# Kernel tuning notes

Hardware: AMD Instinct MI355X
Metric: run time of the kernel (lower is better)

## Reference

```python
import jax, jax.numpy as jnp
import numpy as np

# Dimensions (see shape_source): batch, tokens, input dim, attention feature dim, output dim
B, T, D_IN, D_ATTN, D_OUT = 8, 2048, 512, 8, 512
# Weight scale keeps Q,K entries ~N(0, 0.5^2) so scores**power stays finite in fp32
W_SCALE = 0.5 / np.sqrt(D_IN)


def setup_inputs() -> dict:
    key = jax.random.key(0)
    k1, k2, k3, k4 = jax.random.split(key, 4)
    Input = jax.random.normal(k1, (B, T, D_IN), dtype=jnp.float32)
    W_q = jax.random.normal(k2, (D_IN, D_ATTN), dtype=jnp.float32) * W_SCALE
    W_k = jax.random.normal(k3, (D_IN, D_ATTN), dtype=jnp.float32) * W_SCALE
    W_v = jax.random.normal(k4, (D_IN, D_OUT), dtype=jnp.float32) * W_SCALE
    return {"Input": Input, "W_q": W_q, "W_k": W_k, "W_v": W_v, "power": D_ATTN}


def reference(Input, W_q, W_k, W_v, power):
    # QKV projections (torch.mm applied per token)
    Q = jnp.einsum('btd,df->btf', Input, W_q)   # [B,T,D_ATTN]
    K = jnp.einsum('btd,df->btf', Input, W_k)   # [B,T,D_ATTN]
    V = jnp.einsum('btd,do->bto', Input, W_v)   # [B,T,D_OUT]
    # Non-standard score transform: elementwise power by Attention.Feature.Num
    scores = jnp.einsum('btf,bsf->bts', Q, K) ** power  # [B,T,T]
    A = jax.nn.softmax(scores, axis=2)
    # Weighted sum of values
    return jnp.einsum('bts,bso->bto', A, V)  # [B,T,D_OUT]
```

## Files before the change

kernel.cpp:

```cpp
#include <hip/hip_runtime.h>
#include <hip/hip_bf16.h>
#include <stdint.h>


typedef float f32x4_t __attribute__((ext_vector_type(4)));
typedef short s16x8_t __attribute__((ext_vector_type(8)));
typedef unsigned int u32;

static __device__ __forceinline__ unsigned short f2bf(float x){
  union { float f; u32 u; } v; v.f = x;
  return (unsigned short)((v.u + 0x7FFFu + ((v.u >> 16) & 1u)) >> 16);
}

static __device__ __forceinline__ u32 pk2bf(float a, float b){
  __hip_bfloat162 h = __float22bfloat162_rn(float2{a, b});
  union { __hip_bfloat162 h2; u32 u; } c; c.h2 = h;
  return c.u;
}

static __device__ __forceinline__ void gload16(const void* g, void* l){
  __builtin_amdgcn_global_load_lds((const __attribute__((address_space(1))) u32*)g,
                                   (__attribute__((address_space(3))) u32*)l, 16, 0, 0);
}

static __device__ __forceinline__ float dot8(const float* q, const float4& a, const float4& b){
  float s = q[0] * a.x;
  s = fmaf(q[1], a.y, s); s = fmaf(q[2], a.z, s); s = fmaf(q[3], a.w, s);
  s = fmaf(q[4], b.x, s); s = fmaf(q[5], b.y, s); s = fmaf(q[6], b.z, s);
  s = fmaf(q[7], b.w, s);
  return s;
}

__global__ __launch_bounds__(256) void k_wvT(const float* __restrict__ Wv,
                                             unsigned short* __restrict__ WvT){
  __shared__ __align__(16) float tile[64][68];
  const int t = threadIdx.x;
  const int dbase = (blockIdx.x >> 3) * 64;
  const int cbase = (blockIdx.x & 7) * 64;
  {
    const int dl = t >> 2, cq = (t & 3) * 16;
    const float* src = Wv + (size_t)(dbase + dl) * 512 + cbase + cq;
#pragma unroll
    for (int i = 0; i < 16; i += 4){
      float4 v = *(const float4*)(src + i);
      tile[dl][cq + i + 0] = v.x; tile[dl][cq + i + 1] = v.y;
      tile[dl][cq + i + 2] = v.z; tile[dl][cq + i + 3] = v.w;
    }
  }
  __syncthreads();
  const int cl = t >> 2, dq = (t & 3) * 16;
  __align__(16) unsigned short o[16];
#pragma unroll
  for (int i = 0; i < 16; ++i) o[i] = f2bf(tile[dq + i][cl]);
  unsigned short* dst = WvT + (size_t)(cbase + cl) * 512 + dbase + dq;
  *(uint4*)dst = *(const uint4*)o;
  *(uint4*)(dst + 8) = *(const uint4*)(o + 8);
}

__global__ __launch_bounds__(256) void k_fused(const float* __restrict__ In,
                                               const float* __restrict__ Wq,
                                               const float* __restrict__ Wk,
                                               const unsigned short* __restrict__ WvT,
                                               float* __restrict__ Qo,
                                               float* __restrict__ Ko,
                                               unsigned short* __restrict__ Vg){
  __shared__ __align__(16) char smem[65536];
  const int t = threadIdx.x;
  if (blockIdx.x < 1024){
    float* wt = (float*)smem;
#pragma unroll
    for (int i = 0; i < 16; i += 4){
      float4 vq = *(const float4*)(Wq + t * 16 + i);
      float4 vk = *(const float4*)(Wk + t * 16 + i);
      const float* pq = &vq.x;
      const float* pk = &vk.x;
#pragma unroll
      for (int j = 0; j < 4; ++j){
        int flat = t * 16 + i + j;
        int d = flat >> 3, f = flat & 7;
        wt[f * 512 + ((((d >> 2) ^ f) << 2) | (d & 3))] = pq[j];
        int fk = f + 8;
        wt[fk * 512 + ((((d >> 2) ^ (fk & 7)) << 2) | (d & 3))] = pk[j];
      }
    }
    __syncthreads();
    const int tok = (int)blockIdx.x * 16 + (t >> 4);
    const int f = t & 15;
    const float* inrow = In + (size_t)tok * 512;
    const float* wrow = &wt[f * 512];
    const int swz = f & 7;
    double acc = 0.0;
    for (int cb = 0; cb < 128; cb += 8){
      float part = 0.f;
#pragma unroll
      for (int c = cb; c < cb + 8; ++c){
        float4 x = *(const float4*)(inrow + c * 4);
        float4 ww = *(const float4*)(wrow + ((c ^ swz) << 2));
        part = fmaf(x.x, ww.x, part); part = fmaf(x.y, ww.y, part);
        part = fmaf(x.z, ww.z, part); part = fmaf(x.w, ww.w, part);
      }
      acc += (double)part;
    }
    float r = (float)acc;
    if (f < 8) Qo[(size_t)tok * 8 + f] = r;
    else       Ko[(size_t)tok * 8 + (f - 8)] = r;
    return;
  }
  char* Ab = smem;
  char* Bb = smem + 16384;
  char* Img = smem + 32768;
  const int vb = (int)blockIdx.x - 1024;
  const int w = t >> 6, lane = t & 63;
  const int mt = vb >> 2, nt = vb & 3;
  const int wm = w >> 1, wn = w & 1;
  const int asub = lane & 3;
  int arow[2], acr[2];
#pragma unroll
  for (int i = 0; i < 2; ++i){
    arow[i] = (w * 2 + i) * 16 + (lane >> 2);
    acr[i]  = asub ^ ((arow[i] >> 1) & 3);
  }
  f32x4_t acc[4][4];
#pragma unroll
  for (int m = 0; m < 4; ++m)
#pragma unroll
    for (int n = 0; n < 4; ++n)
      acc[m][n] = (f32x4_t){0.f, 0.f, 0.f, 0.f};

  auto stageB = [&](int kk, int sel){
#pragma unroll
    for (int i = 0; i < 2; ++i){
      int id = w * 2 + i;
      const unsigned short* gb = WvT + (size_t)(nt * 128 + arow[i]) * 512 + kk * 32 + acr[i] * 8;
      gload16(gb, Bb + sel * 8192 + id * 1024);
    }
  };
  auto loadA = [&](int kk, float4* x, float4* y){
#pragma unroll
    for (int i = 0; i < 2; ++i){
      const float* ga = In + (size_t)(mt * 128 + arow[i]) * 512 + kk * 32 + acr[i] * 8;
      x[i] = *(const float4*)ga;
      y[i] = *(const float4*)(ga + 4);
    }
  };
  auto writeA = [&](const float4* x, const float4* y, int sel){
#pragma unroll
    for (int i = 0; i < 2; ++i){
      __align__(16) unsigned short pk[8] = {
        f2bf(x[i].x), f2bf(x[i].y), f2bf(x[i].z), f2bf(x[i].w),
        f2bf(y[i].x), f2bf(y[i].y), f2bf(y[i].z), f2bf(y[i].w)};
      *(uint4*)(Ab + sel * 8192 + arow[i] * 64 + asub * 16) = *(const uint4*)pk;
    }
  };
  {
    float4 x[2], y[2];
    loadA(0, x, y);
    stageB(0, 0);
    writeA(x, y, 0);
    __syncthreads();
  }
  for (int kk = 0; kk < 16; ++kk){
    const int cur = kk & 1;
    float4 x[2], y[2];
    if (kk < 15){
      loadA(kk + 1, x, y);
      stageB(kk + 1, cur ^ 1);
    }
    s16x8_t a[4], bf[4];
#pragma unroll
    for (int m = 0; m < 4; ++m){
      int row = wm * 64 + m * 16 + (lane & 15);
      int chn = (lane >> 4) ^ ((row >> 1) & 3);
      a[m] = *(const s16x8_t*)(Ab + cur * 8192 + row * 64 + chn * 16);
    }
#pragma unroll
    for (int n = 0; n < 4; ++n){
      int col = wn * 64 + n * 16 + (lane & 15);
      int chn = (lane >> 4) ^ ((col >> 1) & 3);
      bf[n] = *(const s16x8_t*)(Bb + cur * 8192 + col * 64 + chn * 16);
    }
#pragma unroll
    for (int m = 0; m < 4; ++m)
#pragma unroll
      for (int n = 0; n < 4; ++n)
        acc[m][n] = __builtin_amdgcn_mfma_f32_16x16x32_bf16(a[m], bf[n], acc[m][n], 0, 0, 0);
    if (kk < 15) writeA(x, y, cur ^ 1);
    __syncthreads();
  }
#pragma unroll
  for (int m = 0; m < 4; ++m){
    const int ks2 = (wm * 2 + (m >> 1)) & 3;
    const int hi  = (m * 2 + ((lane >> 4) >> 1)) & 3;
    const int lo0 = ((lane >> 4) & 1) * 4;
#pragma unroll
    for (int n = 0; n < 4; ++n){
      const int g_loc = wn * 2 + (n >> 1);
      const int n2 = n & 1;
      const int cl = lane & 15;
      __align__(8) unsigned short pk2[4];
#pragma unroll
      for (int j = 0; j < 4; ++j) pk2[j] = f2bf(acc[m][n][j]);
      int boff = g_loc * 8192 + n2 * 4096 + ks2 * 1024 + hi * 256 + cl * 16 + lo0 * 2;
      *(uint2*)(Img + boff) = *(const uint2*)pk2;
    }
  }
  __syncthreads();
  const int bq = mt >> 4;
  const int kt = mt & 15;
#pragma unroll
  for (int i = 0; i < 8; ++i){
    int G = i * 256 + t;
    unsigned short* dst = Vg + (size_t)bq * 1048576 + (size_t)kt * 65536
                        + nt * 16384 + G * 8;
    *(uint4*)dst = *(const uint4*)(Img + G * 16);
  }
}

__global__ __launch_bounds__(1024) void k_attn(const float* __restrict__ Qg,
                                               const float* __restrict__ Kg,
                                               const unsigned short* __restrict__ Vg,
                                               float* __restrict__ Out){
  __shared__ __align__(16) char smem[102656];
  const int t = threadIdx.x;
  const int g = t >> 6, lane = t & 63;
  const int b = blockIdx.x & 7;
  const int qt = blockIdx.x >> 3;
  const int qbase = qt * 64;

  float qreg[8];
  {
    const float* Qp = Qg + (size_t)(b * 2048 + qbase + lane) * 8;
    float4 a = *(const float4*)Qp;
    float4 c = *(const float4*)(Qp + 4);
    qreg[0] = a.x; qreg[1] = a.y; qreg[2] = a.z; qreg[3] = a.w;
    qreg[4] = c.x; qreg[5] = c.y; qreg[6] = c.z; qreg[7] = c.w;
  }
  const float* Kp = Kg + (size_t)b * (2048 * 8);
  const unsigned short* Vb = Vg + (size_t)b * 1048576;
  char* Klds = smem;
  char* Pb = smem + 65536;
  float* red = (float*)(smem + 98304);
  float* fin = (float*)(smem + 102400);

#pragma unroll
  for (int i = 0; i < 4; ++i)
    gload16(Kp + (size_t)(i * 1024 + t) * 4, Klds + (i * 1024 + t) * 16);
  __syncthreads();

  float amax = 0.f;
  {
    const float* kbase = (const float*)Klds + (g * 8) * 8;
#pragma unroll 2
    for (int tt = 0; tt < 16; ++tt){
      const float* kb = kbase + tt * 1024;
#pragma unroll
      for (int j = 0; j < 8; ++j){
        float4 k0 = *(const float4*)(kb + j * 8);
        float4 k1 = *(const float4*)(kb + j * 8 + 4);
        amax = fmaxf(amax, fabsf(dot8(qreg, k0, k1)));
      }
    }
  }
  red[g * 64 + lane] = amax;
  __syncthreads();
  float am = red[lane];
#pragma unroll
  for (int s = 1; s < 16; ++s) am = fmaxf(am, red[s * 64 + lane]);
  float mreg;
  { float s2 = am * am; float s4 = s2 * s2; mreg = s4 * s4; }
  const float LOG2E = 1.44269504f;
  const float me2 = mreg * LOG2E;
  float lp = 0.f;

  const int pswz = ((g ^ (lane & 15)) << 4);
  auto score = [&](int tt, int sel){
    const float* kb = (const float*)Klds + (tt * 128 + g * 8) * 8;
    float es[8];
#pragma unroll
    for (int j = 0; j < 8; ++j){
      float4 k0 = *(const float4*)(kb + j * 8);
      float4 k1 = *(const float4*)(kb + j * 8 + 4);
      float s = dot8(qreg, k0, k1);
      float s2 = s * s; float s4 = s2 * s2; float p = s4 * s4;
      es[j] = exp2f(fmaf(p, LOG2E, -me2));
      lp += es[j];
    }
    uint4 pkd;
    pkd.x = pk2bf(es[0], es[1]); pkd.y = pk2bf(es[2], es[3]);
    pkd.z = pk2bf(es[4], es[5]); pkd.w = pk2bf(es[6], es[7]);
    *(uint4*)(Pb + sel * 16384 + lane * 256 + pswz) = pkd;
  };

  f32x4_t acc[4][2];
#pragma unroll
  for (int mm = 0; mm < 4; ++mm)
#pragma unroll
    for (int n = 0; n < 2; ++n)
      acc[mm][n] = (f32x4_t){0.f, 0.f, 0.f, 0.f};

  score(0, 0);
  __syncthreads();

  for (int tt = 0; tt < 16; ++tt){
    const int sel = tt & 1;
    s16x8_t vf[2][4];
    {
      const unsigned short* vb = Vb + (size_t)tt * 65536 + g * 4096 + lane * 8;
#pragma unroll
      for (int n = 0; n < 2; ++n)
#pragma unroll
        for (int ks = 0; ks < 4; ++ks)
          vf[n][ks] = *(const s16x8_t*)(vb + n * 2048 + ks * 512);
    }
    if (tt + 1 < 16) score(tt + 1, sel ^ 1);
#pragma unroll
    for (int ks = 0; ks < 4; ++ks){
      s16x8_t a[4];
#pragma unroll
      for (int mm = 0; mm < 4; ++mm){
        int r = mm * 16 + (lane & 15);
        int slot = (ks * 4 + (lane >> 4)) ^ (r & 15);
        a[mm] = *(const s16x8_t*)(Pb + sel * 16384 + r * 256 + (slot << 4));
      }
      __builtin_amdgcn_s_setprio(1);
#pragma unroll
      for (int mm = 0; mm < 4; ++mm)
#pragma unroll
        for (int n = 0; n < 2; ++n)
          acc[mm][n] = __builtin_amdgcn_mfma_f32_16x16x32_bf16(a[mm], vf[n][ks], acc[mm][n], 0, 0, 0);
      __builtin_amdgcn_s_setprio(0);
    }
    __syncthreads();
  }

  red[g * 64 + lane] = lp;
  __syncthreads();
  if (t < 64){
    float s = red[t];
#pragma unroll
    for (int s2 = 1; s2 < 16; ++s2) s += red[s2 * 64 + t];
    fin[t] = 1.f / s;
  }
  __syncthreads();

  float* img = (float*)smem;
#pragma unroll
  for (int mm = 0; mm < 4; ++mm){
    float linv[4];
#pragma unroll
    for (int j = 0; j < 4; ++j)
      linv[j] = fin[mm * 16 + ((lane >> 4) << 2) + j];
#pragma unroll
    for (int n = 0; n < 2; ++n){
      int colL = g * 32 + n * 16 + (lane & 15);
#pragma unroll
      for (int j = 0; j < 4; ++j){
        int r16 = ((lane >> 4) << 2) + j;
        img[r16 * 520 + colL] = acc[mm][n][j] * linv[j];
      }
    }
    __syncthreads();
#pragma unroll
    for (int i = 0; i < 2; ++i){
      int f4 = i * 1024 + t;
      int r16 = f4 >> 7, c4 = f4 & 127;
      float4 v = *(const float4*)(img + r16 * 520 + c4 * 4);
      *(float4*)(Out + (size_t)(b * 2048 + qbase + mm * 16 + r16) * 512 + c4 * 4) = v;
    }
    __syncthreads();
  }
}

extern "C" void kernel_launch(void* const* d_in, const int* in_sizes, int n_in,
                              void* d_out, int out_size, void* d_ws, size_t ws_size,
                              hipStream_t stream){
  const float* In = (const float*)d_in[0];
  const float* Wq = (const float*)d_in[1];
  const float* Wk = (const float*)d_in[2];
  const float* Wv = (const float*)d_in[3];
  char* ws = (char*)d_ws;
  unsigned short* WvT = (unsigned short*)(ws);
  float* Q            = (float*)(ws + 524288);
  float* K            = (float*)(ws + 1048576);
  unsigned short* Vg  = (unsigned short*)(ws + 1572864);
  float* Out = (float*)d_out;

  hipLaunchKernelGGL(k_wvT,   dim3(64),   dim3(256),  0, stream, Wv, WvT);
  hipLaunchKernelGGL(k_fused, dim3(1536), dim3(256),  0, stream, In, Wq, Wk, WvT, Q, K, Vg);
  hipLaunchKernelGGL(k_attn,  dim3(256),  dim3(1024), 0, stream, Q, K, Vg, Out);
}
```

Baseline: 102.5 us.

## Double-buffer V fragment loads across tiles and stage input rows in LDS

The attention loop now prefetches the next tile's V fragments into a second register buffer, unrolled by two, so global V loads overlap the current tile's MFMA work instead of being issued right before it. The QK projection blocks copy their 16 input rows into LDS asynchronously and compute from there instead of reading global memory per thread. The max-score pass tracks s*s instead of |s|, which saves one squaring later. More live vector registers may lower occupancy.

```diff
diff --git a/kernel.cpp b/kernel.cpp
--- a/kernel.cpp
+++ b/kernel.cpp
@@ -68,6 +68,11 @@
   const int t = threadIdx.x;
   if (blockIdx.x < 1024){
     float* wt = (float*)smem;
+    float* inT = (float*)(smem + 32768);
+    const float* Inb = In + (size_t)blockIdx.x * 16 * 512;
+#pragma unroll
+    for (int i = 0; i < 8; ++i)
+      gload16(Inb + (i * 256 + t) * 4, (char*)inT + (i * 256 + t) * 16);
 #pragma unroll
     for (int i = 0; i < 16; i += 4){
       float4 vq = *(const float4*)(Wq + t * 16 + i);
@@ -84,9 +89,9 @@
       }
     }
     __syncthreads();
-    const int tok = (int)blockIdx.x * 16 + (t >> 4);
+    const int tokl = t >> 4;
     const int f = t & 15;
-    const float* inrow = In + (size_t)tok * 512;
+    const float* inrow = inT + tokl * 512;
     const float* wrow = &wt[f * 512];
     const int swz = f & 7;
     double acc = 0.0;
@@ -102,6 +107,7 @@
       acc += (double)part;
     }
     float r = (float)acc;
+    const int tok = (int)blockIdx.x * 16 + tokl;
     if (f < 8) Qo[(size_t)tok * 8 + f] = r;
     else       Ko[(size_t)tok * 8 + (f - 8)] = r;
     return;
@@ -247,7 +253,7 @@
     gload16(Kp + (size_t)(i * 1024 + t) * 4, Klds + (i * 1024 + t) * 16);
   __syncthreads();
 
-  float amax = 0.f;
+  float amax2 = 0.f;
   {
     const float* kbase = (const float*)Klds + (g * 8) * 8;
 #pragma unroll 2
@@ -257,17 +263,18 @@
       for (int j = 0; j < 8; ++j){
         float4 k0 = *(const float4*)(kb + j * 8);
         float4 k1 = *(const float4*)(kb + j * 8 + 4);
-        amax = fmaxf(amax, fabsf(dot8(qreg, k0, k1)));
+        float s = dot8(qreg, k0, k1);
+        amax2 = fmaxf(amax2, s * s);
       }
     }
   }
-  red[g * 64 + lane] = amax;
+  red[g * 64 + lane] = amax2;
   __syncthreads();
   float am = red[lane];
 #pragma unroll
   for (int s = 1; s < 16; ++s) am = fmaxf(am, red[s * 64 + lane]);
   float mreg;
-  { float s2 = am * am; float s4 = s2 * s2; mreg = s4 * s4; }
+  { float s4 = am * am; mreg = s4 * s4; }
   const float LOG2E = 1.44269504f;
   const float me2 = mreg * LOG2E;
   float lp = 0.f;
@@ -291,6 +298,15 @@
     *(uint4*)(Pb + sel * 16384 + lane * 256 + pswz) = pkd;
   };
 
+  auto vload = [&](int tt, s16x8_t vf[2][4]){
+    const unsigned short* vb = Vb + (size_t)tt * 65536 + g * 4096 + lane * 8;
+#pragma unroll
+    for (int n = 0; n < 2; ++n)
+#pragma unroll
+      for (int ks = 0; ks < 4; ++ks)
+        vf[n][ks] = *(const s16x8_t*)(vb + n * 2048 + ks * 512);
+  };
+
   f32x4_t acc[4][2];
 #pragma unroll
   for (int mm = 0; mm < 4; ++mm)
@@ -298,21 +314,7 @@
     for (int n = 0; n < 2; ++n)
       acc[mm][n] = (f32x4_t){0.f, 0.f, 0.f, 0.f};
 
-  score(0, 0);
-  __syncthreads();
-
-  for (int tt = 0; tt < 16; ++tt){
-    const int sel = tt & 1;
-    s16x8_t vf[2][4];
-    {
-      const unsigned short* vb = Vb + (size_t)tt * 65536 + g * 4096 + lane * 8;
-#pragma unroll
-      for (int n = 0; n < 2; ++n)
-#pragma unroll
-        for (int ks = 0; ks < 4; ++ks)
-          vf[n][ks] = *(const s16x8_t*)(vb + n * 2048 + ks * 512);
-    }
-    if (tt + 1 < 16) score(tt + 1, sel ^ 1);
+  auto mfma_tile = [&](int sel, s16x8_t vf[2][4]){
 #pragma unroll
     for (int ks = 0; ks < 4; ++ks){
       s16x8_t a[4];
@@ -330,6 +332,24 @@
           acc[mm][n] = __builtin_amdgcn_mfma_f32_16x16x32_bf16(a[mm], vf[n][ks], acc[mm][n], 0, 0, 0);
       __builtin_amdgcn_s_setprio(0);
     }
+  };
+
+  score(0, 0);
+  s16x8_t vfA[2][4], vfB[2][4];
+  vload(0, vfA);
+  __syncthreads();
+
+  for (int it = 0; it < 8; ++it){
+    const int t0 = it * 2, t1 = it * 2 + 1;
+    vload(t1, vfB);
+    if (t0 + 1 < 16) score(t0 + 1, 1);
+    mfma_tile(0, vfA);
+    __syncthreads();
+    if (t1 + 1 < 16){
+      vload(t1 + 1, vfA);
+      score(t1 + 1, 0);
+    }
+    mfma_tile(1, vfB);
     __syncthreads();
   }
 
```

After: 122.6 us. 1.2x slower.

## Remap attention score work: each wave owns 4 query rows, K stored transposed

Applied to the files above, without the earlier changes.

K is now written in a key-interleaved transposed layout so that in the attention kernel each wave handles 4 query rows and each lane scores 2 keys per tile. Row max and row sum reductions become wave shuffles instead of LDS round trips and block barriers. Score computation is split across the ks loop so it interleaves with the MFMAs. The Q/K projection also stages its input rows into LDS with async global-to-LDS loads. The cost is more Q registers and a more complex K scatter in the projection kernel.

```diff
diff --git a/kernel.cpp b/kernel.cpp
--- a/kernel.cpp
+++ b/kernel.cpp
@@ -62,12 +62,17 @@
                                                const float* __restrict__ Wk,
                                                const unsigned short* __restrict__ WvT,
                                                float* __restrict__ Qo,
-                                               float* __restrict__ Ko,
+                                               float* __restrict__ Kt,
                                                unsigned short* __restrict__ Vg){
   __shared__ __align__(16) char smem[65536];
   const int t = threadIdx.x;
   if (blockIdx.x < 1024){
     float* wt = (float*)smem;
+    float* inT = (float*)(smem + 32768);
+    const float* Inb = In + (size_t)blockIdx.x * 16 * 512;
+#pragma unroll
+    for (int i = 0; i < 8; ++i)
+      gload16(Inb + (i * 256 + t) * 4, (char*)inT + (i * 256 + t) * 16);
 #pragma unroll
     for (int i = 0; i < 16; i += 4){
       float4 vq = *(const float4*)(Wq + t * 16 + i);
@@ -84,9 +89,9 @@
       }
     }
     __syncthreads();
-    const int tok = (int)blockIdx.x * 16 + (t >> 4);
+    const int tokl = t >> 4;
     const int f = t & 15;
-    const float* inrow = In + (size_t)tok * 512;
+    const float* inrow = inT + tokl * 512;
     const float* wrow = &wt[f * 512];
     const int swz = f & 7;
     double acc = 0.0;
@@ -102,8 +107,14 @@
       acc += (double)part;
     }
     float r = (float)acc;
+    const int tok = (int)blockIdx.x * 16 + tokl;
     if (f < 8) Qo[(size_t)tok * 8 + f] = r;
-    else       Ko[(size_t)tok * 8 + (f - 8)] = r;
+    else {
+      const int bq = tok >> 11, kk = tok & 2047;
+      const int key = kk & 127, d = f - 8;
+      Kt[(size_t)bq * 16384 + (size_t)(kk >> 7) * 1024
+         + ((key & 1) * 2 + (d >> 2)) * 256 + (key >> 1) * 4 + (d & 3)] = r;
+    }
     return;
   }
   char* Ab = smem;
@@ -217,7 +228,7 @@
 }
 
 __global__ __launch_bounds__(1024) void k_attn(const float* __restrict__ Qg,
-                                               const float* __restrict__ Kg,
+                                               const float* __restrict__ Kt,
                                                const unsigned short* __restrict__ Vg,
                                                float* __restrict__ Out){
   __shared__ __align__(16) char smem[102656];
@@ -227,19 +238,19 @@
   const int qt = blockIdx.x >> 3;
   const int qbase = qt * 64;
 
-  float qreg[8];
-  {
-    const float* Qp = Qg + (size_t)(b * 2048 + qbase + lane) * 8;
+  float q4[4][8];
+#pragma unroll
+  for (int rr = 0; rr < 4; ++rr){
+    const float* Qp = Qg + (size_t)(b * 2048 + qbase + g * 4 + rr) * 8;
     float4 a = *(const float4*)Qp;
     float4 c = *(const float4*)(Qp + 4);
-    qreg[0] = a.x; qreg[1] = a.y; qreg[2] = a.z; qreg[3] = a.w;
-    qreg[4] = c.x; qreg[5] = c.y; qreg[6] = c.z; qreg[7] = c.w;
-  }
-  const float* Kp = Kg + (size_t)b * (2048 * 8);
+    q4[rr][0] = a.x; q4[rr][1] = a.y; q4[rr][2] = a.z; q4[rr][3] = a.w;
+    q4[rr][4] = c.x; q4[rr][5] = c.y; q4[rr][6] = c.z; q4[rr][7] = c.w;
+  }
+  const float* Kp = Kt + (size_t)b * 16384;
   const unsigned short* Vb = Vg + (size_t)b * 1048576;
   char* Klds = smem;
   char* Pb = smem + 65536;
-  float* red = (float*)(smem + 98304);
   float* fin = (float*)(smem + 102400);
 
 #pragma unroll
@@ -247,49 +258,50 @@
     gload16(Kp + (size_t)(i * 1024 + t) * 4, Klds + (i * 1024 + t) * 16);
   __syncthreads();
 
-  float amax = 0.f;
+  float mx0 = 0.f, mx1 = 0.f, mx2 = 0.f, mx3 = 0.f;
   {
-    const float* kbase = (const float*)Klds + (g * 8) * 8;
+    const float* kbase = (const float*)Klds + lane * 4;
 #pragma unroll 2
     for (int tt = 0; tt < 16; ++tt){
       const float* kb = kbase + tt * 1024;
-#pragma unroll
-      for (int j = 0; j < 8; ++j){
-        float4 k0 = *(const float4*)(kb + j * 8);
-        float4 k1 = *(const float4*)(kb + j * 8 + 4);
-        amax = fmaxf(amax, fabsf(dot8(qreg, k0, k1)));
-      }
-    }
-  }
-  red[g * 64 + lane] = amax;
-  __syncthreads();
-  float am = red[lane];
-#pragma unroll
-  for (int s = 1; s < 16; ++s) am = fmaxf(am, red[s * 64 + lane]);
-  float mreg;
-  { float s2 = am * am; float s4 = s2 * s2; mreg = s4 * s4; }
+      float4 r0 = *(const float4*)(kb);
+      float4 r1 = *(const float4*)(kb + 256);
+      float4 r2 = *(const float4*)(kb + 512);
+      float4 r3 = *(const float4*)(kb + 768);
+      {
+        float s0 = dot8(q4[0], r0, r1), s1 = dot8(q4[0], r2, r3);
+        mx0 = fmaxf(mx0, fmaxf(s0 * s0, s1 * s1));
+      }
+      {
+        float s0 = dot8(q4[1], r0, r1), s1 = dot8(q4[1], r2, r3);
+        mx1 = fmaxf(mx1, fmaxf(s0 * s0, s1 * s1));
+      }
+      {
+        float s0 = dot8(q4[2], r0, r1), s1 = dot8(q4[2], r2, r3);
+        mx2 = fmaxf(mx2, fmaxf(s0 * s0, s1 * s1));
+      }
+      {
+        float s0 = dot8(q4[3], r0, r1), s1 = dot8(q4[3], r2, r3);
+        mx3 = fmaxf(mx3, fmaxf(s0 * s0, s1 * s1));
+      }
+    }
+  }
+#pragma unroll
+  for (int sh = 1; sh < 64; sh <<= 1){
+    mx0 = fmaxf(mx0, __shfl_xor(mx0, sh));
+    mx1 = fmaxf(mx1, __shfl_xor(mx1, sh));
+    mx2 = fmaxf(mx2, __shfl_xor(mx2, sh));
+    mx3 = fmaxf(mx3, __shfl_xor(mx3, sh));
+  }
   const float LOG2E = 1.44269504f;
-  const float me2 = mreg * LOG2E;
-  float lp = 0.f;
-
-  const int pswz = ((g ^ (lane & 15)) << 4);
-  auto score = [&](int tt, int sel){
-    const float* kb = (const float*)Klds + (tt * 128 + g * 8) * 8;
-    float es[8];
-#pragma unroll
-    for (int j = 0; j < 8; ++j){
-      float4 k0 = *(const float4*)(kb + j * 8);
-      float4 k1 = *(const float4*)(kb + j * 8 + 4);
-      float s = dot8(qreg, k0, k1);
-      float s2 = s * s; float s4 = s2 * s2; float p = s4 * s4;
-      es[j] = exp2f(fmaf(p, LOG2E, -me2));
-      lp += es[j];
-    }
-    uint4 pkd;
-    pkd.x = pk2bf(es[0], es[1]); pkd.y = pk2bf(es[2], es[3]);
-    pkd.z = pk2bf(es[4], es[5]); pkd.w = pk2bf(es[6], es[7]);
-    *(uint4*)(Pb + sel * 16384 + lane * 256 + pswz) = pkd;
-  };
+  float nme2_0, nme2_1, nme2_2, nme2_3;
+  { float s4 = mx0 * mx0; nme2_0 = -(s4 * s4) * LOG2E; }
+  { float s4 = mx1 * mx1; nme2_1 = -(s4 * s4) * LOG2E; }
+  { float s4 = mx2 * mx2; nme2_2 = -(s4 * s4) * LOG2E; }
+  { float s4 = mx3 * mx3; nme2_3 = -(s4 * s4) * LOG2E; }
+  float lp0 = 0.f, lp1 = 0.f, lp2 = 0.f, lp3 = 0.f;
+
+  const int pwoff = (((lane >> 2)) << 4) + (lane & 3) * 4;
 
   f32x4_t acc[4][2];
 #pragma unroll
@@ -298,7 +310,32 @@
     for (int n = 0; n < 2; ++n)
       acc[mm][n] = (f32x4_t){0.f, 0.f, 0.f, 0.f};
 
-  score(0, 0);
+  auto scoreRow = [&](int rr, float nme2r, float& lpr,
+                      const float4& r0, const float4& r1,
+                      const float4& r2, const float4& r3, int sel){
+    float s0 = dot8(q4[rr], r0, r1), s1 = dot8(q4[rr], r2, r3);
+    float p0, p1;
+    { float a2 = s0 * s0; float a4 = a2 * a2; p0 = a4 * a4; }
+    { float a2 = s1 * s1; float a4 = a2 * a2; p1 = a4 * a4; }
+    float e0 = __builtin_amdgcn_exp2f(fmaf(p0, LOG2E, nme2r));
+    float e1 = __builtin_amdgcn_exp2f(fmaf(p1, LOG2E, nme2r));
+    lpr += e0 + e1;
+    const int row = g * 4 + rr;
+    *(u32*)(Pb + sel * 16384 + row * 256
+            + ((((lane >> 2) ^ (row & 15))) << 4) + (lane & 3) * 4) = pk2bf(e0, e1);
+  };
+
+  {
+    const float* kb = (const float*)Klds + lane * 4;
+    float4 r0 = *(const float4*)(kb);
+    float4 r1 = *(const float4*)(kb + 256);
+    float4 r2 = *(const float4*)(kb + 512);
+    float4 r3 = *(const float4*)(kb + 768);
+    scoreRow(0, nme2_0, lp0, r0, r1, r2, r3, 0);
+    scoreRow(1, nme2_1, lp1, r0, r1, r2, r3, 0);
+    scoreRow(2, nme2_2, lp2, r0, r1, r2, r3, 0);
+    scoreRow(3, nme2_3, lp3, r0, r1, r2, r3, 0);
+  }
   __syncthreads();
 
   for (int tt = 0; tt < 16; ++tt){
@@ -312,9 +349,23 @@
         for (int ks = 0; ks < 4; ++ks)
           vf[n][ks] = *(const s16x8_t*)(vb + n * 2048 + ks * 512);
     }
-    if (tt + 1 < 16) score(tt + 1, sel ^ 1);
+    const bool more = (tt + 1 < 16);
+    float4 r0, r1, r2, r3;
+    if (more){
+      const float* kb = (const float*)Klds + ((tt + 1) & 15) * 1024 + lane * 4;
+      r0 = *(const float4*)(kb);
+      r1 = *(const float4*)(kb + 256);
+      r2 = *(const float4*)(kb + 512);
+      r3 = *(const float4*)(kb + 768);
+    }
 #pragma unroll
     for (int ks = 0; ks < 4; ++ks){
+      if (more){
+        if (ks == 0) scoreRow(0, nme2_0, lp0, r0, r1, r2, r3, sel ^ 1);
+        if (ks == 1) scoreRow(1, nme2_1, lp1, r0, r1, r2, r3, sel ^ 1);
+        if (ks == 2) scoreRow(2, nme2_2, lp2, r0, r1, r2, r3, sel ^ 1);
+        if (ks == 3) scoreRow(3, nme2_3, lp3, r0, r1, r2, r3, sel ^ 1);
+      }
       s16x8_t a[4];
 #pragma unroll
       for (int mm = 0; mm < 4; ++mm){
@@ -333,13 +384,18 @@
     __syncthreads();
   }
 
-  red[g * 64 + lane] = lp;
-  __syncthreads();
-  if (t < 64){
-    float s = red[t];
-#pragma unroll
-    for (int s2 = 1; s2 < 16; ++s2) s += red[s2 * 64 + t];
-    fin[t] = 1.f / s;
+#pragma unroll
+  for (int sh = 1; sh < 64; sh <<= 1){
+    lp0 += __shfl_xor(lp0, sh);
+    lp1 += __shfl_xor(lp1, sh);
+    lp2 += __shfl_xor(lp2, sh);
+    lp3 += __shfl_xor(lp3, sh);
+  }
+  if (lane == 0){
+    fin[g * 4 + 0] = 1.f / lp0;
+    fin[g * 4 + 1] = 1.f / lp1;
+    fin[g * 4 + 2] = 1.f / lp2;
+    fin[g * 4 + 3] = 1.f / lp3;
   }
   __syncthreads();
 
@@ -381,11 +437,11 @@
   char* ws = (char*)d_ws;
   unsigned short* WvT = (unsigned short*)(ws);
   float* Q            = (float*)(ws + 524288);
-  float* K            = (float*)(ws + 1048576);
+  float* Kt           = (float*)(ws + 1048576);
   unsigned short* Vg  = (unsigned short*)(ws + 1572864);
   float* Out = (float*)d_out;
 
   hipLaunchKernelGGL(k_wvT,   dim3(64),   dim3(256),  0, stream, Wv, WvT);
-  hipLaunchKernelGGL(k_fused, dim3(1536), dim3(256),  0, stream, In, Wq, Wk, WvT, Q, K, Vg);
-  hipLaunchKernelGGL(k_attn,  dim3(256),  dim3(1024), 0, stream, Q, K, Vg, Out);
-}
+  hipLaunchKernelGGL(k_fused, dim3(1536), dim3(256),  0, stream, In, Wq, Wk, WvT, Q, Kt, Vg);
+  hipLaunchKernelGGL(k_attn,  dim3(256),  dim3(1024), 0, stream, Q, Kt, Vg, Out);
+}
```

Measured after the change: 118.6 us. 1.16x slower.
